# Optimization experiments

Hardware: AMD Instinct MI355X
Metric: run time of the kernel (lower is better)

Reference implementation:

```python
import jax, jax.numpy as jnp
import numpy as np

IN0, OUT0 = 64, 64   # layer 0: input_size -> hidden
IN1, OUT1 = 64, 16   # layer 1: hidden -> output_size
H = 2                # subnetwork hidden width (subnetwork_shape=[2,2])
BATCH = 16384


def _make_layer_params(key, n_subnets):
    ks = jax.random.split(key, 6)
    s1 = 1.0  # fan_in=1
    s2 = 1.0 / np.sqrt(H)
    W1 = jax.random.uniform(ks[0], (n_subnets, H, 1), minval=-s1, maxval=s1)
    b1 = jax.random.uniform(ks[1], (n_subnets, H), minval=-s1, maxval=s1)
    W2 = jax.random.uniform(ks[2], (n_subnets, H, H), minval=-s2, maxval=s2)
    b2 = jax.random.uniform(ks[3], (n_subnets, H), minval=-s2, maxval=s2)
    W3 = jax.random.uniform(ks[4], (n_subnets, 1, H), minval=-s2, maxval=s2)
    b3 = jax.random.uniform(ks[5], (n_subnets, 1), minval=-s2, maxval=s2)
    return W1, b1, W2, b2, W3, b3


def setup_inputs() -> dict:
    key = jax.random.key(0)
    kx, k0, k1 = jax.random.split(key, 3)
    x = jax.random.normal(kx, (BATCH, IN0), dtype=jnp.float32)
    l0 = _make_layer_params(k0, IN0 * OUT0)
    l1 = _make_layer_params(k1, IN1 * OUT1)
    names = ['W1', 'b1', 'W2', 'b2', 'W3', 'b3']
    inp = {'x': x}
    for n, v in zip(names, l0):
        inp['l0_' + n] = v
    for n, v in zip(names, l1):
        inp['l1_' + n] = v
    return inp


def _kan_layer(x, in_size, out_size, W1, b1, W2, b2, W3, b3):
    # x: [B, in] -> x_expanded: [in*out, B, 1]; subnet n = i*out + o
    B = x.shape[0]
    xe = jnp.repeat(x.T, out_size, axis=0)[:, :, None]          # [N, B, 1]
    h = jax.nn.relu(jnp.einsum('nbi,nhi->nbh', xe, W1) + b1[:, None, :])  # [N, B, H]
    h = jax.nn.relu(jnp.einsum('nbh,nkh->nbk', h, W2) + b2[:, None, :])   # [N, B, H]
    o = jnp.einsum('nbk,nok->nbo', h, W3) + b3[:, None, :]                # [N, B, 1]
    o = o[..., 0].reshape(in_size, out_size, B).sum(axis=0)               # [out, B]
    return o.T                                                            # [B, out]


def reference(x, l0_W1, l0_b1, l0_W2, l0_b2, l0_W3, l0_b3,
              l1_W1, l1_b1, l1_W2, l1_b2, l1_W3, l1_b3):
    h = _kan_layer(x, IN0, OUT0, l0_W1, l0_b1, l0_W2, l0_b2, l0_W3, l0_b3)
    out = _kan_layer(h, IN1, OUT1, l1_W1, l1_b1, l1_W2, l1_b2, l1_W3, l1_b3)
    return out
```

## Files before the change

kernel.cpp:

```cpp
#include <hip/hip_runtime.h>


typedef float v2f __attribute__((ext_vector_type(2)));

#define BATCH 16384
#define TB    64

#define OW1 0
#define OB1 1024
#define OW2 2048
#define OB2 4096
#define OW3 5120
#define OB3 6144
#define WBUF_F 6656

__device__ __forceinline__ void copy16(float* __restrict__ dst,
                                       const float* __restrict__ src,
                                       int nbytes, int t) {
#pragma unroll 1
    for (int k = t * 16; k < nbytes; k += 512 * 16) {
        const float4 v = *(const float4*)((const char*)src + k);
        *(float4*)((char*)dst + k) = v;
    }
}

__device__ __forceinline__ void stage_chunk(float* wbuf,
    const float* W1, const float* b1, const float* W2,
    const float* b2, const float* W3, const float* b3,
    int s0, int t) {
    copy16(wbuf + OW1, W1 + 2 * s0, 4096, t);
    copy16(wbuf + OB1, b1 + 2 * s0, 4096, t);
    copy16(wbuf + OW2, W2 + 4 * s0, 8192, t);
    copy16(wbuf + OB2, b2 + 2 * s0, 4096, t);
    copy16(wbuf + OW3, W3 + 2 * s0, 4096, t);
    copy16(wbuf + OB3, b3 + s0,     2048, t);
}

__global__ __launch_bounds__(512) void kan_fused(
    const float* __restrict__ x,
    const float* __restrict__ A1, const float* __restrict__ a1,
    const float* __restrict__ A2, const float* __restrict__ a2,
    const float* __restrict__ A3, const float* __restrict__ a3,
    const float* __restrict__ B1, const float* __restrict__ c1,
    const float* __restrict__ B2, const float* __restrict__ c2,
    const float* __restrict__ B3, const float* __restrict__ c3,
    float* __restrict__ out)
{
    __shared__ float xs[64][68];
    __shared__ float ht[64][68];
    __shared__ float wbuf[WBUF_F];

    const int t    = threadIdx.x;
    const int lane = t & 63;
    const int wave = t >> 6;
    const int boff = 8 * wave;
    const int bB0  = blockIdx.x * TB;

#pragma unroll 1
    for (int k = t * 4; k < TB * 64; k += 512 * 4) {
        const float4 v = *(const float4*)(x + (long)bB0 * 64 + k);
        const int b = k >> 6, i = k & 63;
        xs[i][b] = v.x; xs[i + 1][b] = v.y; xs[i + 2][b] = v.z; xs[i + 3][b] = v.w;
    }
    stage_chunk(wbuf, A1, a1, A2, a2, A3, a3, 0, t);
    __syncthreads();

    const v2f zz = {0.f, 0.f};

    const int o = lane;
    v2f acc[4] = {zz, zz, zz, zz};
    float bsum = 0.f;

#pragma unroll 1
    for (int c = 0; c < 8; ++c) {
#pragma unroll 2
        for (int ic = 0; ic < 8; ++ic) {
            const int i = 8 * c + ic;
            const int n = (ic << 6) + o;
            const v2f    w1 = *(const v2f*)(wbuf + OW1 + 2 * n);
            const v2f    d1 = *(const v2f*)(wbuf + OB1 + 2 * n);
            const float4 w2 = *(const float4*)(wbuf + OW2 + 4 * n);
            const v2f    d2 = *(const v2f*)(wbuf + OB2 + 2 * n);
            const v2f    w3 = *(const v2f*)(wbuf + OW3 + 2 * n);
            bsum += wbuf[OB3 + n];

            const v2f W1X = {w1.x, w1.x}, W1Y = {w1.y, w1.y};
            const v2f D1X = {d1.x, d1.x}, D1Y = {d1.y, d1.y};
            const v2f W2X = {w2.x, w2.x}, W2Y = {w2.y, w2.y};
            const v2f W2Z = {w2.z, w2.z}, W2W = {w2.w, w2.w};
            const v2f D2X = {d2.x, d2.x}, D2Y = {d2.y, d2.y};
            const v2f W3X = {w3.x, w3.x}, W3Y = {w3.y, w3.y};

            const float4 xv0 = *(const float4*)&xs[i][boff];
            const float4 xv1 = *(const float4*)&xs[i][boff + 4];
            const float4 xq[2] = {xv0, xv1};
            const v2f* xp = (const v2f*)xq;

#pragma unroll
            for (int jp = 0; jp < 4; ++jp) {
                v2f m0 = __builtin_elementwise_fma(xp[jp], W1X, D1X);
                v2f m1 = __builtin_elementwise_fma(xp[jp], W1Y, D1Y);
                m0 = __builtin_elementwise_max(m0, zz);
                m1 = __builtin_elementwise_max(m1, zz);
                v2f t0 = __builtin_elementwise_fma(W2Y, m1, D2X);
                t0 = __builtin_elementwise_fma(W2X, m0, t0);
                v2f t1 = __builtin_elementwise_fma(W2W, m1, D2Y);
                t1 = __builtin_elementwise_fma(W2Z, m0, t1);
                t0 = __builtin_elementwise_max(t0, zz);
                t1 = __builtin_elementwise_max(t1, zz);
                acc[jp] = __builtin_elementwise_fma(W3X, t0, acc[jp]);
                acc[jp] = __builtin_elementwise_fma(W3Y, t1, acc[jp]);
            }
        }
        __syncthreads();
        if (c < 7) stage_chunk(wbuf, A1, a1, A2, a2, A3, a3, 512 * (c + 1), t);
        else       stage_chunk(wbuf, B1, c1, B2, c2, B3, c3, 0, t);
        __syncthreads();
    }

#pragma unroll
    for (int jp = 0; jp < 4; ++jp) {
        ht[o][boff + 2 * jp]     = acc[jp].x + bsum;
        ht[o][boff + 2 * jp + 1] = acc[jp].y + bsum;
    }
    __syncthreads();

    const int o1 = lane & 15;
    const int bg = lane >> 4;
    const int bp = boff + 2 * bg;
    v2f accA = zz, accB = zz;
    float bsum1 = 0.f;

#pragma unroll 1
    for (int cc = 0; cc < 2; ++cc) {
#pragma unroll 4
        for (int ii = 0; ii < 32; ++ii) {
            const int i = 32 * cc + ii;
            const int n = (ii << 4) + o1;
            const v2f    w1 = *(const v2f*)(wbuf + OW1 + 2 * n);
            const v2f    d1 = *(const v2f*)(wbuf + OB1 + 2 * n);
            const float4 w2 = *(const float4*)(wbuf + OW2 + 4 * n);
            const v2f    d2 = *(const v2f*)(wbuf + OB2 + 2 * n);
            const v2f    w3 = *(const v2f*)(wbuf + OW3 + 2 * n);
            bsum1 += wbuf[OB3 + n];

            const v2f W1X = {w1.x, w1.x}, W1Y = {w1.y, w1.y};
            const v2f D1X = {d1.x, d1.x}, D1Y = {d1.y, d1.y};
            const v2f W2X = {w2.x, w2.x}, W2Y = {w2.y, w2.y};
            const v2f W2Z = {w2.z, w2.z}, W2W = {w2.w, w2.w};
            const v2f D2X = {d2.x, d2.x}, D2Y = {d2.y, d2.y};
            const v2f W3X = {w3.x, w3.x}, W3Y = {w3.y, w3.y};

            const v2f hv = *(const v2f*)&ht[i][bp];

            v2f m0 = __builtin_elementwise_fma(hv, W1X, D1X);
            v2f m1 = __builtin_elementwise_fma(hv, W1Y, D1Y);
            m0 = __builtin_elementwise_max(m0, zz);
            m1 = __builtin_elementwise_max(m1, zz);
            v2f t0 = __builtin_elementwise_fma(W2Y, m1, D2X);
            t0 = __builtin_elementwise_fma(W2X, m0, t0);
            v2f t1 = __builtin_elementwise_fma(W2W, m1, D2Y);
            t1 = __builtin_elementwise_fma(W2Z, m0, t1);
            t0 = __builtin_elementwise_max(t0, zz);
            t1 = __builtin_elementwise_max(t1, zz);
            if (ii & 1) {
                accB = __builtin_elementwise_fma(W3X, t0, accB);
                accB = __builtin_elementwise_fma(W3Y, t1, accB);
            } else {
                accA = __builtin_elementwise_fma(W3X, t0, accA);
                accA = __builtin_elementwise_fma(W3Y, t1, accA);
            }
        }
        __syncthreads();
        if (cc == 0) {
            stage_chunk(wbuf, B1, c1, B2, c2, B3, c3, 512, t);
            __syncthreads();
        }
    }

    const v2f r = accA + accB;
    out[(long)(bB0 + bp) * 16 + o1]     = r.x + bsum1;
    out[(long)(bB0 + bp + 1) * 16 + o1] = r.y + bsum1;
}

extern "C" void kernel_launch(void* const* d_in, const int* in_sizes, int n_in,
                              void* d_out, int out_size, void* d_ws, size_t ws_size,
                              hipStream_t stream) {
    const float* x     = (const float*)d_in[0];
    const float* l0_W1 = (const float*)d_in[1];
    const float* l0_b1 = (const float*)d_in[2];
    const float* l0_W2 = (const float*)d_in[3];
    const float* l0_b2 = (const float*)d_in[4];
    const float* l0_W3 = (const float*)d_in[5];
    const float* l0_b3 = (const float*)d_in[6];
    const float* l1_W1 = (const float*)d_in[7];
    const float* l1_b1 = (const float*)d_in[8];
    const float* l1_W2 = (const float*)d_in[9];
    const float* l1_b2 = (const float*)d_in[10];
    const float* l1_W3 = (const float*)d_in[11];
    const float* l1_b3 = (const float*)d_in[12];

    float* outp = (float*)d_out;

    dim3 blk(512);
    dim3 grid(BATCH / TB);
    hipLaunchKernelGGL(kan_fused, grid, blk, 0, stream,
                       x,
                       l0_W1, l0_b1, l0_W2, l0_b2, l0_W3, l0_b3,
                       l1_W1, l1_b1, l1_W2, l1_b2, l1_W3, l1_b3,
                       outp);
}
```

Before: 114.4 us.

## Split input dimension across wave pairs with wider per-thread batch tiles

Each wave now covers 16 batch rows instead of 8, and pairs of waves split each chunk's input features in half. Each thread therefore amortises every shared-memory weight load over twice as many batch elements. Partial hidden sums go to two shared buffers, with the x buffer reused as the second one. Layer 1 splits inputs across lane groups and reduces them with cross-lane shuffles, then writes coalesced float4 output through shared memory. The changes also set a launch-bounds minimum of two blocks per CU. This adds register pressure, an extra reduction, and a shared-memory round trip for the output.

```diff
diff --git a/kernel.cpp b/kernel.cpp
--- a/kernel.cpp
+++ b/kernel.cpp
@@ -36,7 +36,7 @@
     copy16(wbuf + OB3, b3 + s0,     2048, t);
 }
 
-__global__ __launch_bounds__(512) void kan_fused(
+__global__ __launch_bounds__(512, 2) void kan_fused(
     const float* __restrict__ x,
     const float* __restrict__ A1, const float* __restrict__ a1,
     const float* __restrict__ A2, const float* __restrict__ a2,
@@ -46,14 +46,19 @@
     const float* __restrict__ B3, const float* __restrict__ c3,
     float* __restrict__ out)
 {
-    __shared__ float xs[64][68];
-    __shared__ float ht[64][68];
+    __shared__ float xsb[64][68];
+    __shared__ float hpA[64][68];
     __shared__ float wbuf[WBUF_F];
+
+    float (*xs)[68]  = xsb;
+    float (*hpB)[68] = xsb;
 
     const int t    = threadIdx.x;
     const int lane = t & 63;
     const int wave = t >> 6;
-    const int boff = 8 * wave;
+    const int ih   = wave & 1;
+    const int bq   = wave >> 1;
+    const int boff = 16 * bq;
     const int bB0  = blockIdx.x * TB;
 
 #pragma unroll 1
@@ -68,15 +73,18 @@
     const v2f zz = {0.f, 0.f};
 
     const int o = lane;
-    v2f acc[4] = {zz, zz, zz, zz};
+    v2f acc[8];
+#pragma unroll
+    for (int j = 0; j < 8; ++j) acc[j] = zz;
     float bsum = 0.f;
 
 #pragma unroll 1
-    for (int c = 0; c < 8; ++c) {
+    for (int p = 0; p < 8; ++p) {
 #pragma unroll 2
-        for (int ic = 0; ic < 8; ++ic) {
-            const int i = 8 * c + ic;
-            const int n = (ic << 6) + o;
+        for (int ii = 0; ii < 4; ++ii) {
+            const int li = 4 * ih + ii;
+            const int gi = 8 * p + li;
+            const int n  = (li << 6) + o;
             const v2f    w1 = *(const v2f*)(wbuf + OW1 + 2 * n);
             const v2f    d1 = *(const v2f*)(wbuf + OB1 + 2 * n);
             const float4 w2 = *(const float4*)(wbuf + OW2 + 4 * n);
@@ -91,13 +99,15 @@
             const v2f D2X = {d2.x, d2.x}, D2Y = {d2.y, d2.y};
             const v2f W3X = {w3.x, w3.x}, W3Y = {w3.y, w3.y};
 
-            const float4 xv0 = *(const float4*)&xs[i][boff];
-            const float4 xv1 = *(const float4*)&xs[i][boff + 4];
-            const float4 xq[2] = {xv0, xv1};
+            const float4 xv0 = *(const float4*)&xs[gi][boff];
+            const float4 xv1 = *(const float4*)&xs[gi][boff + 4];
+            const float4 xv2 = *(const float4*)&xs[gi][boff + 8];
+            const float4 xv3 = *(const float4*)&xs[gi][boff + 12];
+            const float4 xq[4] = {xv0, xv1, xv2, xv3};
             const v2f* xp = (const v2f*)xq;
 
 #pragma unroll
-            for (int jp = 0; jp < 4; ++jp) {
+            for (int jp = 0; jp < 8; ++jp) {
                 v2f m0 = __builtin_elementwise_fma(xp[jp], W1X, D1X);
                 v2f m1 = __builtin_elementwise_fma(xp[jp], W1Y, D1Y);
                 m0 = __builtin_elementwise_max(m0, zz);
@@ -113,30 +123,35 @@
             }
         }
         __syncthreads();
-        if (c < 7) stage_chunk(wbuf, A1, a1, A2, a2, A3, a3, 512 * (c + 1), t);
+        if (p < 7) stage_chunk(wbuf, A1, a1, A2, a2, A3, a3, 512 * (p + 1), t);
         else       stage_chunk(wbuf, B1, c1, B2, c2, B3, c3, 0, t);
         __syncthreads();
     }
 
-#pragma unroll
-    for (int jp = 0; jp < 4; ++jp) {
-        ht[o][boff + 2 * jp]     = acc[jp].x + bsum;
-        ht[o][boff + 2 * jp + 1] = acc[jp].y + bsum;
+    {
+        float (*hp)[68] = ih ? hpB : hpA;
+#pragma unroll
+        for (int jp = 0; jp < 8; ++jp) {
+            hp[o][boff + 2 * jp]     = acc[jp].x + bsum;
+            hp[o][boff + 2 * jp + 1] = acc[jp].y + bsum;
+        }
     }
     __syncthreads();
 
     const int o1 = lane & 15;
-    const int bg = lane >> 4;
-    const int bp = boff + 2 * bg;
-    v2f accA = zz, accB = zz;
+    const int ig = lane >> 4;
+    v2f acc1[8];
+#pragma unroll
+    for (int j = 0; j < 8; ++j) acc1[j] = zz;
     float bsum1 = 0.f;
 
 #pragma unroll 1
-    for (int cc = 0; cc < 2; ++cc) {
-#pragma unroll 4
-        for (int ii = 0; ii < 32; ++ii) {
-            const int i = 32 * cc + ii;
-            const int n = (ii << 4) + o1;
+    for (int q = 0; q < 2; ++q) {
+#pragma unroll 2
+        for (int s = 0; s < 4; ++s) {
+            const int li = 16 * ih + 4 * s + ig;
+            const int gi = 32 * q + li;
+            const int n  = (li << 4) + o1;
             const v2f    w1 = *(const v2f*)(wbuf + OW1 + 2 * n);
             const v2f    d1 = *(const v2f*)(wbuf + OB1 + 2 * n);
             const float4 w2 = *(const float4*)(wbuf + OW2 + 4 * n);
@@ -151,36 +166,68 @@
             const v2f D2X = {d2.x, d2.x}, D2Y = {d2.y, d2.y};
             const v2f W3X = {w3.x, w3.x}, W3Y = {w3.y, w3.y};
 
-            const v2f hv = *(const v2f*)&ht[i][bp];
-
-            v2f m0 = __builtin_elementwise_fma(hv, W1X, D1X);
-            v2f m1 = __builtin_elementwise_fma(hv, W1Y, D1Y);
-            m0 = __builtin_elementwise_max(m0, zz);
-            m1 = __builtin_elementwise_max(m1, zz);
-            v2f t0 = __builtin_elementwise_fma(W2Y, m1, D2X);
-            t0 = __builtin_elementwise_fma(W2X, m0, t0);
-            v2f t1 = __builtin_elementwise_fma(W2W, m1, D2Y);
-            t1 = __builtin_elementwise_fma(W2Z, m0, t1);
-            t0 = __builtin_elementwise_max(t0, zz);
-            t1 = __builtin_elementwise_max(t1, zz);
-            if (ii & 1) {
-                accB = __builtin_elementwise_fma(W3X, t0, accB);
-                accB = __builtin_elementwise_fma(W3Y, t1, accB);
-            } else {
-                accA = __builtin_elementwise_fma(W3X, t0, accA);
-                accA = __builtin_elementwise_fma(W3Y, t1, accA);
+            v2f hv[8];
+#pragma unroll
+            for (int m = 0; m < 4; ++m) {
+                const float4 av = *(const float4*)&hpA[gi][boff + 4 * m];
+                const float4 bv = *(const float4*)&hpB[gi][boff + 4 * m];
+                hv[2 * m]     = v2f{av.x + bv.x, av.y + bv.y};
+                hv[2 * m + 1] = v2f{av.z + bv.z, av.w + bv.w};
             }
+
+#pragma unroll
+            for (int jp = 0; jp < 8; ++jp) {
+                v2f m0 = __builtin_elementwise_fma(hv[jp], W1X, D1X);
+                v2f m1 = __builtin_elementwise_fma(hv[jp], W1Y, D1Y);
+                m0 = __builtin_elementwise_max(m0, zz);
+                m1 = __builtin_elementwise_max(m1, zz);
+                v2f t0 = __builtin_elementwise_fma(W2Y, m1, D2X);
+                t0 = __builtin_elementwise_fma(W2X, m0, t0);
+                v2f t1 = __builtin_elementwise_fma(W2W, m1, D2Y);
+                t1 = __builtin_elementwise_fma(W2Z, m0, t1);
+                t0 = __builtin_elementwise_max(t0, zz);
+                t1 = __builtin_elementwise_max(t1, zz);
+                acc1[jp] = __builtin_elementwise_fma(W3X, t0, acc1[jp]);
+                acc1[jp] = __builtin_elementwise_fma(W3Y, t1, acc1[jp]);
+            }
         }
         __syncthreads();
-        if (cc == 0) {
+        if (q == 0) {
             stage_chunk(wbuf, B1, c1, B2, c2, B3, c3, 512, t);
             __syncthreads();
         }
     }
 
-    const v2f r = accA + accB;
-    out[(long)(bB0 + bp) * 16 + o1]     = r.x + bsum1;
-    out[(long)(bB0 + bp + 1) * 16 + o1] = r.y + bsum1;
+#pragma unroll
+    for (int jp = 0; jp < 8; ++jp) {
+        float vx = acc1[jp].x, vy = acc1[jp].y;
+        vx += __shfl_xor(vx, 16, 64); vx += __shfl_xor(vx, 32, 64);
+        vy += __shfl_xor(vy, 16, 64); vy += __shfl_xor(vy, 32, 64);
+        acc1[jp].x = vx; acc1[jp].y = vy;
+    }
+    bsum1 += __shfl_xor(bsum1, 16, 64);
+    bsum1 += __shfl_xor(bsum1, 32, 64);
+
+    float* opA = wbuf;
+    float* opB = wbuf + 1024;
+    if (ig == 0) {
+        float* op = ih ? opB : opA;
+#pragma unroll
+        for (int jp = 0; jp < 8; ++jp) {
+            op[(boff + 2 * jp) * 16 + o1]     = acc1[jp].x + bsum1;
+            op[(boff + 2 * jp + 1) * 16 + o1] = acc1[jp].y + bsum1;
+        }
+    }
+    __syncthreads();
+
+    if (t < 256) {
+        const int f = t * 4;
+        const float4 u = *(const float4*)(opA + f);
+        const float4 v = *(const float4*)(opB + f);
+        float4 r;
+        r.x = u.x + v.x; r.y = u.y + v.y; r.z = u.z + v.z; r.w = u.w + v.w;
+        *(float4*)(out + (long)bB0 * 16 + f) = r;
+    }
 }
 
 extern "C" void kernel_launch(void* const* d_in, const int* in_sizes, int n_in,
```

Result: no change. 114.3 us (-0.2%).
